# Performance work log

Measured on AMD Instinct MI355X. Metric: run time of the kernel, lower is better.

## Reference

```python
import jax, jax.numpy as jnp
import numpy as np

B, H, W, C, NH, K = 1, 64, 64, 384, 6, 7
DH = C // NH
EPS = 1e-6


def setup_inputs() -> dict:
    key = jax.random.key(0)
    ks = jax.random.split(key, 8)
    s = 0.02
    return {
        "x": jax.random.normal(ks[0], (B, H * W, C), jnp.float32),
        "cond": jax.random.normal(ks[1], (B, C), jnp.float32),
        "qkv_w": jax.random.normal(ks[2], (C, 3 * C), jnp.float32) * s,
        "qkv_b": jnp.zeros((3 * C,), jnp.float32),
        "proj_w": jax.random.normal(ks[3], (C, C), jnp.float32) * s,
        "proj_b": jnp.zeros((C,), jnp.float32),
        "fc1_w": jax.random.normal(ks[4], (C, 4 * C), jnp.float32) * s,
        "fc1_b": jnp.zeros((4 * C,), jnp.float32),
        "fc2_w": jax.random.normal(ks[5], (4 * C, C), jnp.float32) * s,
        "fc2_b": jnp.zeros((C,), jnp.float32),
        "ada_w": jax.random.normal(ks[6], (C, 6 * C), jnp.float32) * s,
        "ada_b": jnp.zeros((6 * C,), jnp.float32),
    }


def _ln(x):
    # LayerNorm with elementwise_affine=False, eps=1e-6
    mu = jnp.mean(x, axis=-1, keepdims=True)
    var = jnp.mean(jnp.square(x - mu), axis=-1, keepdims=True)
    return (x - mu) / jnp.sqrt(var + EPS)


def _win_idx(n):
    # NATTEN boundary-clamped window: start = clip(i - K//2, 0, n-K)
    starts = jnp.clip(jnp.arange(n) - K // 2, 0, n - K)
    return starts[:, None] + jnp.arange(K)[None, :]  # [n, K]


def _natten(y, qkv_w, qkv_b, proj_w, proj_b):
    # y: [B, H, W, C] -> neighborhood attention with 7x7 clamped windows
    qkv = y @ qkv_w + qkv_b
    q, k, v = jnp.split(qkv, 3, axis=-1)
    q = q.reshape(B, H, W, NH, DH) * (DH ** -0.5)
    k = k.reshape(B, H, W, NH, DH)
    v = v.reshape(B, H, W, NH, DH)
    ih = _win_idx(H)  # [H, K]
    iw = _win_idx(W)  # [W, K]
    kw = k[:, ih][:, :, :, iw]  # [B, H, K, W, K, NH, DH]
    vw = v[:, ih][:, :, :, iw]  # [B, H, K, W, K, NH, DH]
    a = jnp.einsum('bxynd,bxiyjnd->bxynij', q, kw)  # [B,H,W,NH,K,K]
    p = jax.nn.softmax(a.reshape(B, H, W, NH, K * K), axis=-1)
    p = p.reshape(B, H, W, NH, K, K)
    o = jnp.einsum('bxynij,bxiyjnd->bxynd', p, vw).reshape(B, H, W, C)
    return o @ proj_w + proj_b


def reference(x, cond, qkv_w, qkv_b, proj_w, proj_b,
              fc1_w, fc1_b, fc2_w, fc2_b, ada_w, ada_b):
    m = jax.nn.silu(cond) @ ada_w + ada_b  # [B, 6C]
    sh_a, sc_a, g_a, sh_m, sc_m, g_m = jnp.split(m, 6, axis=-1)
    # attention branch
    y = _ln(x) * (1.0 + sc_a[:, None]) + sh_a[:, None]
    z = _natten(y.reshape(B, H, W, C), qkv_w, qkv_b, proj_w, proj_b)
    x = x + g_a[:, None] * z.reshape(B, H * W, C)
    # mlp branch
    y = _ln(x) * (1.0 + sc_m[:, None]) + sh_m[:, None]
    hdn = jax.nn.gelu(y @ fc1_w + fc1_b, approximate=True)
    x = x + g_m[:, None] * (hdn @ fc2_w + fc2_b)
    return x
```

## Files before the change

### kernel.cpp

```cpp
#include <hip/hip_runtime.h>
#include <hip/hip_bf16.h>
#include <math.h>

#define GH 64
#define GW 64
#define CC 384
#define NHD 6
#define KW 7
#define DH 64
#define NTOK (GH*GW)
#define LN_EPS 1e-6f

typedef __attribute__((ext_vector_type(4))) float f32x4;
typedef __attribute__((ext_vector_type(8))) short bf16x8;
typedef __hip_bfloat16 bf16;

typedef const __attribute__((address_space(1))) unsigned int* gptr_t;
typedef __attribute__((address_space(3))) unsigned int* lptr_t;

__device__ __forceinline__ float bf2f(unsigned int u16) {
    union { unsigned int i; float f; } c; c.i = u16 << 16; return c.f;
}
__device__ __forceinline__ bf16 f2bf(float f) { return __float2bfloat16(f); }

__global__ __launch_bounds__(256) void wt_ada_k(const float* __restrict__ qkv_w,
                                                const float* __restrict__ proj_w,
                                                const float* __restrict__ fc1_w,
                                                const float* __restrict__ fc2_w,
                                                bf16* __restrict__ qkv_wt,
                                                bf16* __restrict__ proj_wt,
                                                bf16* __restrict__ fc1_wt,
                                                bf16* __restrict__ fc2_wt,
                                                const float* __restrict__ cond,
                                                const float* __restrict__ aw,
                                                const float* __restrict__ ab,
                                                float* __restrict__ m)
{
    int b = blockIdx.x;
    int tid = threadIdx.x;
    if (b >= 432) {
        __shared__ float s[CC];
        __shared__ float red[4][64];
        for (int i = tid; i < CC; i += 256) {
            float c = cond[i];
            s[i] = c / (1.f + __expf(-c));
        }
        __syncthreads();
        int c  = tid & 63;
        int ks = tid >> 6;
        int col = (b - 432) * 64 + c;
        float acc = 0.f;
        for (int k = ks * 96; k < (ks + 1) * 96; ++k)
            acc += s[k] * aw[(size_t)k * (6*CC) + col];
        red[ks][c] = acc;
        __syncthreads();
        if (tid < 64)
            m[col] = red[0][c] + red[1][c] + red[2][c] + red[3][c] + ab[col];
        return;
    }
    __shared__ float t[64][65];
    const float* in; bf16* outp; int K, N, lid;
    if (b < 108)       { in = qkv_w;  outp = qkv_wt;  K = 384;  N = 1152; lid = b; }
    else if (b < 144)  { in = proj_w; outp = proj_wt; K = 384;  N = 384;  lid = b - 108; }
    else if (b < 288)  { in = fc1_w;  outp = fc1_wt;  K = 384;  N = 1536; lid = b - 144; }
    else               { in = fc2_w;  outp = fc2_wt;  K = 1536; N = 384;  lid = b - 288; }
    int nbn = N >> 6;
    int bn = (lid % nbn) << 6, bk = (lid / nbn) << 6;
    int c4 = (tid & 15) * 4, r0 = tid >> 4;
    #pragma unroll
    for (int p = 0; p < 4; ++p) {
        int r = r0 + p * 16;
        float4 v = *(const float4*)&in[(size_t)(bk + r) * N + bn + c4];
        t[r][c4+0] = v.x; t[r][c4+1] = v.y; t[r][c4+2] = v.z; t[r][c4+3] = v.w;
    }
    __syncthreads();
    #pragma unroll
    for (int p = 0; p < 4; ++p) {
        int n = r0 + p * 16;
        ushort4 w;
        w.x = __bfloat16_as_ushort(f2bf(t[c4+0][n]));
        w.y = __bfloat16_as_ushort(f2bf(t[c4+1][n]));
        w.z = __bfloat16_as_ushort(f2bf(t[c4+2][n]));
        w.w = __bfloat16_as_ushort(f2bf(t[c4+3][n]));
        *(ushort4*)&outp[(size_t)(bn + n) * K + bk + c4] = w;
    }
}

__global__ __launch_bounds__(128) void ln_mod_k(const float* __restrict__ xin,
                                                const float* __restrict__ sh,
                                                const float* __restrict__ sc,
                                                bf16* __restrict__ yout)
{
    int t = blockIdx.x;
    int tid = threadIdx.x;
    const float* xr = xin + (size_t)t * CC;
    float v0 = xr[tid], v1 = xr[tid + 128], v2 = xr[tid + 256];
    float s  = v0 + v1 + v2;
    float ss = v0*v0 + v1*v1 + v2*v2;
    #pragma unroll
    for (int off = 32; off; off >>= 1) {
        s  += __shfl_down(s,  off);
        ss += __shfl_down(ss, off);
    }
    __shared__ float red[4];
    int wid = tid >> 6;
    if ((tid & 63) == 0) { red[wid*2] = s; red[wid*2+1] = ss; }
    __syncthreads();
    s  = red[0] + red[2];
    ss = red[1] + red[3];
    float mean = s * (1.f / CC);
    float var  = ss * (1.f / CC) - mean * mean;
    float rstd = rsqrtf(var + LN_EPS);
    bf16* yr = yout + (size_t)t * CC;
    yr[tid      ] = f2bf((v0 - mean) * rstd * (1.f + sc[tid      ]) + sh[tid      ]);
    yr[tid + 128] = f2bf((v1 - mean) * rstd * (1.f + sc[tid + 128]) + sh[tid + 128]);
    yr[tid + 256] = f2bf((v2 - mean) * rstd * (1.f + sc[tid + 256]) + sh[tid + 256]);
}

#define GBK 64

template<int EPI, typename OutT, int BM, int BN, int TPB, int DEPTH>
__global__ __launch_bounds__(TPB) void mgemm_k(const bf16* __restrict__ A,
                                               const bf16* __restrict__ Bt,
                                               const float* __restrict__ bias,
                                               const float* __restrict__ resid,
                                               const float* __restrict__ gvec,
                                               OutT* __restrict__ out,
                                               int M, int N, int Kd)
{
    constexpr int WR = 2, WC = TPB / 128;
    constexpr int FM = BM / WR / 16, FN = BN / WC / 16;
    constexpr int RPP = TPB / 8;
    constexpr int PA = BM / RPP > 0 ? BM / RPP : 1;
    constexpr int PB = BN / RPP > 0 ? BN / RPP : 1;
    constexpr int LDST = PA + PB;
    constexpr int STAGE_BYTES = DEPTH * (BM + BN) * GBK * 2;
    constexpr int EPI_BYTES = (EPI == 1) ? BM * (BN + 4) * 4 : BM * (BN + 8) * 2;
    constexpr int SMEM = STAGE_BYTES > EPI_BYTES ? STAGE_BYTES : EPI_BYTES;
    __shared__ __align__(16) char smem[SMEM];
    bf16* As = (bf16*)smem;
    bf16* Bs = (bf16*)(smem + DEPTH * BM * GBK * 2);

    int tid = threadIdx.x;
    int wid = tid >> 6, lane = tid & 63;
    int wm = wid / WC, wn = wid % WC;

    int gx = gridDim.x;
    int nwg = gx * gridDim.y;
    int bid = blockIdx.y * gx + blockIdx.x;
    int swz = (bid & 7) * (nwg >> 3) + (bid >> 3);
    int bx = swz % gx, by = swz / gx;

    int row_base = by * BM;
    int col_base = bx * BN;

    int l8 = lane >> 3;
    int cs = ((lane & 7) ^ l8) * 8;
    int xr = (lane & 7) << 4;
    int bcol = (lane >> 4) * 16;

    f32x4 acc[FM][FN] = {};
    const int nt = Kd / GBK;

    auto STAGE = [&](int buf, int t) {
        int k0 = t * GBK;
        #pragma unroll
        for (int p = 0; p < PA; ++p) {
            int rb = (p * RPP + wid * 8) % BM;
            __builtin_amdgcn_global_load_lds(
                (gptr_t)(const void*)(A + (size_t)(row_base + rb + l8) * Kd + k0 + cs),
                (lptr_t)(void*)(As + (buf * BM + rb) * GBK), 16, 0, 0);
        }
        #pragma unroll
        for (int p = 0; p < PB; ++p) {
            int rb = (p * RPP + wid * 8) % BN;
            __builtin_amdgcn_global_load_lds(
                (gptr_t)(const void*)(Bt + (size_t)(col_base + rb + l8) * Kd + k0 + cs),
                (lptr_t)(void*)(Bs + (buf * BN + rb) * GBK), 16, 0, 0);
        }
    };

    #pragma unroll
    for (int d = 0; d < DEPTH - 1; ++d) STAGE(d, d);

    int cur = 0;
    for (int t = 0; t < nt; ++t) {
        if (t + DEPTH - 1 < nt)
            STAGE((cur + DEPTH - 1) % DEPTH, t + DEPTH - 1);
        int ahead = min(nt - 1, t + DEPTH - 1) - t;
        if constexpr (DEPTH == 3) {
            if (ahead == 2)      asm volatile("s_waitcnt vmcnt(%0)" :: "n"(2*LDST) : "memory");
            else if (ahead == 1) asm volatile("s_waitcnt vmcnt(%0)" :: "n"(LDST)   : "memory");
            else                 asm volatile("s_waitcnt vmcnt(0)" ::: "memory");
        } else {
            if (ahead == 1)      asm volatile("s_waitcnt vmcnt(%0)" :: "n"(LDST)   : "memory");
            else                 asm volatile("s_waitcnt vmcnt(0)" ::: "memory");
        }
        __builtin_amdgcn_sched_barrier(0);
        __builtin_amdgcn_s_barrier();
        __builtin_amdgcn_sched_barrier(0);
        #pragma unroll
        for (int kk = 0; kk < GBK; kk += 32) {
            bf16x8 af[FM], bfr[FN];
            #pragma unroll
            for (int m = 0; m < FM; ++m) {
                int R = wm*(BM/WR) + m*16 + (lane & 15);
                af[m]  = *(const bf16x8*)((const char*)As + (cur*BM + R)*128 + ((kk*2 + bcol) ^ xr));
            }
            #pragma unroll
            for (int n = 0; n < FN; ++n) {
                int R = wn*(BN/WC) + n*16 + (lane & 15);
                bfr[n] = *(const bf16x8*)((const char*)Bs + (cur*BN + R)*128 + ((kk*2 + bcol) ^ xr));
            }
            #pragma unroll
            for (int m = 0; m < FM; ++m)
                #pragma unroll
                for (int n = 0; n < FN; ++n)
                    acc[m][n] = __builtin_amdgcn_mfma_f32_16x16x32_bf16(af[m], bfr[n], acc[m][n], 0, 0, 0);
        }
        __builtin_amdgcn_sched_barrier(0);
        __builtin_amdgcn_s_barrier();
        __builtin_amdgcn_sched_barrier(0);
        cur = (cur + 1 == DEPTH) ? 0 : cur + 1;
    }

    int cl = lane & 15, rq = lane >> 4;
    if constexpr (EPI == 1) {
        float* et = (float*)smem;
        #pragma unroll
        for (int m = 0; m < FM; ++m)
            #pragma unroll
            for (int n = 0; n < FN; ++n) {
                int col = wn*(BN/WC) + n*16 + cl;
                float bv = bias[col_base + col];
                #pragma unroll
                for (int j = 0; j < 4; ++j) {
                    int row = wm*(BM/WR) + m*16 + rq*4 + j;
                    et[row*(BN+4) + col] = acc[m][n][j] + bv;
                }
            }
        __syncthreads();
        constexpr int CH = BN / 4;
        #pragma unroll
        for (int p = 0; p < (BM*CH)/TPB; ++p) {
            int idx = p * TPB + tid;
            int row = idx / CH, ch = idx % CH;
            float4 v = *(const float4*)&et[row*(BN+4) + ch*4];
            size_t gidx = (size_t)(row_base + row) * N + col_base + ch*4;
            float4 r = *(const float4*)&resid[gidx];
            float4 g = *(const float4*)&gvec[col_base + ch*4];
            float4 o;
            o.x = r.x + g.x * v.x;
            o.y = r.y + g.y * v.y;
            o.z = r.z + g.z * v.z;
            o.w = r.w + g.w * v.w;
            *(float4*)&((float*)out)[gidx] = o;
        }
    } else {
        bf16* et = (bf16*)smem;
        #pragma unroll
        for (int m = 0; m < FM; ++m)
            #pragma unroll
            for (int n = 0; n < FN; ++n) {
                int col = wn*(BN/WC) + n*16 + cl;
                float bv = bias[col_base + col];
                #pragma unroll
                for (int j = 0; j < 4; ++j) {
                    int row = wm*(BM/WR) + m*16 + rq*4 + j;
                    float v = acc[m][n][j] + bv;
                    if constexpr (EPI == 2) {
                        float u = 0.7978845608028654f * (v + 0.044715f * v * v * v);
                        v = v / (1.f + __expf(-2.f * u));
                    }
                    et[row*(BN+8) + col] = f2bf(v);
                }
            }
        __syncthreads();
        constexpr int CH = BN / 8;
        #pragma unroll
        for (int p = 0; p < (BM*CH)/TPB; ++p) {
            int idx = p * TPB + tid;
            int row = idx / CH, ch = idx % CH;
            bf16x8 v = *(const bf16x8*)&et[row*(BN+8) + ch*8];
            *(bf16x8*)&((bf16*)out)[(size_t)(row_base + row) * N + col_base + ch*8] = v;
        }
    }
}

#define QOFF 0
#define KOFF 8192
#define VOFF 36864
#define POFF 65536

__global__ __launch_bounds__(256) void natten_k(const bf16* __restrict__ qkv,
                                                bf16* __restrict__ o)
{
    __shared__ __align__(16) char lds[95232];
    int tid = threadIdx.x;
    int wid = tid >> 6, lane = tid & 63;
    int b = blockIdx.x;
    int h = b % NHD, tile = b / NHD;
    int R0 = (tile >> 3) << 3, C0 = (tile & 7) << 3;
    int wr0 = min(max(R0 - 3, 0), GH - 14);
    int wc0 = min(max(C0 - 3, 0), GW - 14);

    int l8 = lane >> 3, c8 = lane & 7;
    int cs = ((c8 ^ l8) << 3);

    #pragma unroll
    for (int p = 0; p < 2; ++p) {
        int rb = p * 32 + wid * 8;
        int q  = rb + l8;
        int token = (R0 + (q >> 3)) * GW + C0 + (q & 7);
        __builtin_amdgcn_global_load_lds(
            (gptr_t)(const void*)(qkv + (size_t)token * (3*CC) + h * DH + cs),
            (lptr_t)(void*)(lds + QOFF + rb * 128), 16, 0, 0);
    }
    #pragma unroll
    for (int p = 0; p < 7; ++p) {
        int rb = p * 32 + wid * 8;
        int key = rb + l8;
        if (key < 196) {
            int kr = (key * 586) >> 13;
            int kc = key - 14 * kr;
            int token = (wr0 + kr) * GW + wc0 + kc;
            const bf16* base = qkv + (size_t)token * (3*CC) + h * DH + cs;
            __builtin_amdgcn_global_load_lds(
                (gptr_t)(const void*)(base + CC),
                (lptr_t)(void*)(lds + KOFF + rb * 128), 16, 0, 0);
            __builtin_amdgcn_global_load_lds(
                (gptr_t)(const void*)(base + 2*CC),
                (lptr_t)(void*)(lds + VOFF + rb * 128), 16, 0, 0);
        }
    }
    for (int i = tid; i < 896; i += 256)
        *(unsigned int*)(lds + VOFF + 196*128 + i * 4) = 0u;
    for (int i = tid; i < 64*18; i += 256) {
        int row = i / 18, seg = i % 18;
        *(unsigned int*)(lds + POFF + row * 464 + 392 + seg * 4) = 0u;
    }
    __syncthreads();

    int qme = wid * 16 + (lane & 15);
    int qr = R0 + (qme >> 3), qc = C0 + (qme & 7);
    int sh = min(max(qr - 3, 0), GH - KW);
    int sw = min(max(qc - 3, 0), GW - KW);

    bf16x8 bq[2];
    #pragma unroll
    for (int kk = 0; kk < 2; ++kk)
        bq[kk] = *(const bf16x8*)(lds + QOFF + qme * 128 +
                  ((kk * 64 + (lane >> 4) * 16) ^ ((qme & 7) << 4)));

    f32x4 sc[13] = {};
    #pragma unroll
    for (int m = 0; m < 13; ++m) {
        #pragma unroll
        for (int kk = 0; kk < 2; ++kk) {
            int R = m * 16 + (lane & 15);
            bf16x8 af = *(const bf16x8*)(lds + KOFF + R * 128 +
                         ((kk * 64 + (lane >> 4) * 16) ^ ((R & 7) << 4)));
            sc[m] = __builtin_amdgcn_mfma_f32_16x16x32_bf16(af, bq[kk], sc[m], 0, 0, 0);
        }
    }
    float mx = -3e38f;
    #pragma unroll
    for (int m = 0; m < 13; ++m) {
        #pragma unroll
        for (int j = 0; j < 4; ++j) {
            int key = m * 16 + (lane >> 4) * 4 + j;
            int kr = (key * 586) >> 13;
            int kc = key - 14 * kr;
            int kg = wr0 + kr, cg = wc0 + kc;
            bool val = (kg >= sh) && (kg <= sh + 6) && (cg >= sw) && (cg <= sw + 6);
            float s = val ? sc[m][j] * 0.125f : -3e38f;
            sc[m][j] = s;
            mx = fmaxf(mx, s);
        }
    }
    mx = fmaxf(mx, __shfl_xor(mx, 16));
    mx = fmaxf(mx, __shfl_xor(mx, 32));
    float sum = 0.f;
    #pragma unroll
    for (int m = 0; m < 13; ++m)
        #pragma unroll
        for (int j = 0; j < 4; ++j) {
            float e = __expf(sc[m][j] - mx);
            sc[m][j] = e;
            sum += e;
        }
    sum += __shfl_xor(sum, 16);
    sum += __shfl_xor(sum, 32);
    float inv = 1.f / sum;

    #pragma unroll
    for (int m = 0; m < 13; ++m)
        #pragma unroll
        for (int j = 0; j < 4; ++j) {
            int key = m * 16 + (lane >> 4) * 4 + j;
            *(bf16*)(lds + POFF + qme * 464 + key * 2) = f2bf(sc[m][j]);
        }
    asm volatile("s_waitcnt lgkmcnt(0)" ::: "memory");
    __builtin_amdgcn_sched_barrier(0);

    f32x4 oacc[4] = {};
    #pragma unroll
    for (int kk = 0; kk < 7; ++kk) {
        bf16x8 af = *(const bf16x8*)(lds + POFF + qme * 464 + kk * 64 + (lane >> 4) * 16);
        #pragma unroll
        for (int n = 0; n < 4; ++n) {
            int dd = n * 16 + (lane & 15);
            int gch = dd >> 3, dby = (dd & 7) * 2;
            bf16x8 bv;
            #pragma unroll
            for (int j = 0; j < 8; ++j) {
                int key = kk * 32 + (lane >> 4) * 8 + j;
                ((short*)&bv)[j] = *(const short*)(lds + VOFF + key * 128 +
                                    ((gch ^ (key & 7)) << 4) + dby);
            }
            oacc[n] = __builtin_amdgcn_mfma_f32_16x16x32_bf16(af, bv, oacc[n], 0, 0, 0);
        }
    }

    #pragma unroll
    for (int j = 0; j < 4; ++j) {
        int idxq = ((lane >> 4) << 2) + j;
        float iv = __shfl(inv, (lane & 48) | idxq);
        int q2 = wid * 16 + idxq;
        int token = (R0 + (q2 >> 3)) * GW + C0 + (q2 & 7);
        #pragma unroll
        for (int n = 0; n < 4; ++n) {
            int d = n * 16 + (lane & 15);
            o[(size_t)token * CC + h * DH + d] = f2bf(oacc[n][j] * iv);
        }
    }
}

extern "C" void kernel_launch(void* const* d_in, const int* in_sizes, int n_in,
                              void* d_out, int out_size, void* d_ws, size_t ws_size,
                              hipStream_t stream)
{
    const float* x      = (const float*)d_in[0];
    const float* cond   = (const float*)d_in[1];
    const float* qkv_w  = (const float*)d_in[2];
    const float* qkv_b  = (const float*)d_in[3];
    const float* proj_w = (const float*)d_in[4];
    const float* proj_b = (const float*)d_in[5];
    const float* fc1_w  = (const float*)d_in[6];
    const float* fc1_b  = (const float*)d_in[7];
    const float* fc2_w  = (const float*)d_in[8];
    const float* fc2_b  = (const float*)d_in[9];
    const float* ada_w  = (const float*)d_in[10];
    const float* ada_b  = (const float*)d_in[11];
    float* out = (float*)d_out;

    char* p = (char*)d_ws;
    float* m       = (float*)p;            p += 6*CC*sizeof(float);
    bf16* y        = (bf16*)p;             p += (size_t)NTOK*CC*2;
    bf16* qkv      = (bf16*)p;             p += (size_t)NTOK*(3*CC)*2;
    bf16* attn_o   = (bf16*)p;             p += (size_t)NTOK*CC*2;
    bf16* hdn      = (bf16*)p;             p += (size_t)NTOK*(4*CC)*2;
    bf16* qkv_wt   = (bf16*)p;             p += (size_t)(3*CC)*CC*2;
    bf16* proj_wt  = (bf16*)p;             p += (size_t)CC*CC*2;
    bf16* fc1_wt   = (bf16*)p;             p += (size_t)(4*CC)*CC*2;
    bf16* fc2_wt   = (bf16*)p;             p += (size_t)CC*(4*CC)*2;

    const float* sh_a = m;
    const float* sc_a = m + CC;
    const float* g_a  = m + 2*CC;
    const float* sh_m = m + 3*CC;
    const float* sc_m = m + 4*CC;
    const float* g_m  = m + 5*CC;

    wt_ada_k<<<468, 256, 0, stream>>>(qkv_w, proj_w, fc1_w, fc2_w,
                                      qkv_wt, proj_wt, fc1_wt, fc2_wt,
                                      cond, ada_w, ada_b, m);
    ln_mod_k<<<NTOK, 128, 0, stream>>>(x, sh_a, sc_a, y);
    mgemm_k<0, bf16, 64, 128, 256, 2><<<dim3((3*CC)/128, NTOK/64), 256, 0, stream>>>(
        y, qkv_wt, qkv_b, nullptr, nullptr, qkv, NTOK, 3*CC, CC);
    natten_k<<<(NTOK/64)*NHD, 256, 0, stream>>>(qkv, attn_o);
    mgemm_k<1, float, 32, 64, 256, 3><<<dim3(CC/64, NTOK/32), 256, 0, stream>>>(
        attn_o, proj_wt, proj_b, x, g_a, out, NTOK, CC, CC);
    ln_mod_k<<<NTOK, 128, 0, stream>>>(out, sh_m, sc_m, y);
    mgemm_k<2, bf16, 64, 128, 256, 2><<<dim3((4*CC)/128, NTOK/64), 256, 0, stream>>>(
        y, fc1_wt, fc1_b, nullptr, nullptr, hdn, NTOK, 4*CC, CC);
    mgemm_k<1, float, 32, 64, 256, 3><<<dim3(CC/64, NTOK/32), 256, 0, stream>>>(
        hdn, fc2_wt, fc2_b, out, g_m, out, NTOK, CC, 4*CC);
}
```

Measured before the change: 79.84 us.

## Fold first LayerNorm into front kernel and apply adaLN modulation inside GEMM A-loads

The first LayerNorm no longer depends on the adaLN vector, so it now runs inside the weight-transpose/ada kernel as extra blocks, which removes one launch and lets it overlap with the weight conversion. Scale and shift are applied to A fragments in registers inside the qkv and fc1 GEMMs, using a shared-memory copy of the modulation vector. The second LayerNorm now handles two tokens per block. The trade is extra per-fragment bf16 unpack/FMA/repack work in the GEMM inner loop, a second bf16 rounding of the activations, and a redundant double load of the modulation values.

Result: slower. 82.58 us (+3.4%).

```diff
diff --git a/kernel.cpp b/kernel.cpp
--- a/kernel.cpp
+++ b/kernel.cpp
@@ -23,24 +23,55 @@
 }
 __device__ __forceinline__ bf16 f2bf(float f) { return __float2bfloat16(f); }
 
-__global__ __launch_bounds__(256) void wt_ada_k(const float* __restrict__ qkv_w,
-                                                const float* __restrict__ proj_w,
-                                                const float* __restrict__ fc1_w,
-                                                const float* __restrict__ fc2_w,
-                                                bf16* __restrict__ qkv_wt,
-                                                bf16* __restrict__ proj_wt,
-                                                bf16* __restrict__ fc1_wt,
-                                                bf16* __restrict__ fc2_wt,
-                                                const float* __restrict__ cond,
-                                                const float* __restrict__ aw,
-                                                const float* __restrict__ ab,
-                                                float* __restrict__ m)
+__global__ __launch_bounds__(256) void front_k(const float* __restrict__ qkv_w,
+                                               const float* __restrict__ proj_w,
+                                               const float* __restrict__ fc1_w,
+                                               const float* __restrict__ fc2_w,
+                                               bf16* __restrict__ qkv_wt,
+                                               bf16* __restrict__ proj_wt,
+                                               bf16* __restrict__ fc1_wt,
+                                               bf16* __restrict__ fc2_wt,
+                                               const float* __restrict__ cond,
+                                               const float* __restrict__ aw,
+                                               const float* __restrict__ ab,
+                                               float* __restrict__ m,
+                                               const float* __restrict__ x,
+                                               bf16* __restrict__ z)
 {
+    __shared__ float t[64][65];
     int b = blockIdx.x;
     int tid = threadIdx.x;
+    if (b >= 468) {
+        int tok = (b - 468) * 2 + (tid >> 7);
+        int lt  = tid & 127;
+        const float* xr = x + (size_t)tok * CC;
+        float v0 = xr[lt], v1 = xr[lt + 128], v2 = xr[lt + 256];
+        float s  = v0 + v1 + v2;
+        float ss = v0*v0 + v1*v1 + v2*v2;
+        #pragma unroll
+        for (int off = 32; off; off >>= 1) {
+            s  += __shfl_down(s,  off);
+            ss += __shfl_down(ss, off);
+        }
+        float* red = (float*)t;
+        int wid = tid >> 6;
+        if ((tid & 63) == 0) { red[wid*2] = s; red[wid*2+1] = ss; }
+        __syncthreads();
+        int base = (tid >> 7) * 4;
+        s  = red[base+0] + red[base+2];
+        ss = red[base+1] + red[base+3];
+        float mean = s * (1.f / CC);
+        float var  = ss * (1.f / CC) - mean * mean;
+        float rstd = rsqrtf(var + LN_EPS);
+        bf16* zr = z + (size_t)tok * CC;
+        zr[lt      ] = f2bf((v0 - mean) * rstd);
+        zr[lt + 128] = f2bf((v1 - mean) * rstd);
+        zr[lt + 256] = f2bf((v2 - mean) * rstd);
+        return;
+    }
     if (b >= 432) {
-        __shared__ float s[CC];
-        __shared__ float red[4][64];
+        float* s   = (float*)t;
+        float* red = s + CC;
         for (int i = tid; i < CC; i += 256) {
             float c = cond[i];
             s[i] = c / (1.f + __expf(-c));
@@ -52,13 +83,12 @@
         float acc = 0.f;
         for (int k = ks * 96; k < (ks + 1) * 96; ++k)
             acc += s[k] * aw[(size_t)k * (6*CC) + col];
-        red[ks][c] = acc;
+        red[ks*64 + c] = acc;
         __syncthreads();
         if (tid < 64)
-            m[col] = red[0][c] + red[1][c] + red[2][c] + red[3][c] + ab[col];
+            m[col] = red[c] + red[64+c] + red[128+c] + red[192+c] + ab[col];
         return;
     }
-    __shared__ float t[64][65];
     const float* in; bf16* outp; int K, N, lid;
     if (b < 108)       { in = qkv_w;  outp = qkv_wt;  K = 384;  N = 1152; lid = b; }
     else if (b < 144)  { in = proj_w; outp = proj_wt; K = 384;  N = 384;  lid = b - 108; }
@@ -86,15 +116,13 @@
     }
 }
 
-__global__ __launch_bounds__(128) void ln_mod_k(const float* __restrict__ xin,
-                                                const float* __restrict__ sh,
-                                                const float* __restrict__ sc,
-                                                bf16* __restrict__ yout)
+__global__ __launch_bounds__(256) void ln_k(const float* __restrict__ xin,
+                                            bf16* __restrict__ z)
 {
-    int t = blockIdx.x;
-    int tid = threadIdx.x;
-    const float* xr = xin + (size_t)t * CC;
-    float v0 = xr[tid], v1 = xr[tid + 128], v2 = xr[tid + 256];
+    int tok = blockIdx.x * 2 + (threadIdx.x >> 7);
+    int lt  = threadIdx.x & 127;
+    const float* xr = xin + (size_t)tok * CC;
+    float v0 = xr[lt], v1 = xr[lt + 128], v2 = xr[lt + 256];
     float s  = v0 + v1 + v2;
     float ss = v0*v0 + v1*v1 + v2*v2;
     #pragma unroll
@@ -102,29 +130,31 @@
         s  += __shfl_down(s,  off);
         ss += __shfl_down(ss, off);
     }
-    __shared__ float red[4];
-    int wid = tid >> 6;
-    if ((tid & 63) == 0) { red[wid*2] = s; red[wid*2+1] = ss; }
+    __shared__ float red[8];
+    int wid = threadIdx.x >> 6;
+    if ((threadIdx.x & 63) == 0) { red[wid*2] = s; red[wid*2+1] = ss; }
     __syncthreads();
-    s  = red[0] + red[2];
-    ss = red[1] + red[3];
+    int base = (threadIdx.x >> 7) * 4;
+    s  = red[base+0] + red[base+2];
+    ss = red[base+1] + red[base+3];
     float mean = s * (1.f / CC);
     float var  = ss * (1.f / CC) - mean * mean;
     float rstd = rsqrtf(var + LN_EPS);
-    bf16* yr = yout + (size_t)t * CC;
-    yr[tid      ] = f2bf((v0 - mean) * rstd * (1.f + sc[tid      ]) + sh[tid      ]);
-    yr[tid + 128] = f2bf((v1 - mean) * rstd * (1.f + sc[tid + 128]) + sh[tid + 128]);
-    yr[tid + 256] = f2bf((v2 - mean) * rstd * (1.f + sc[tid + 256]) + sh[tid + 256]);
+    bf16* zr = z + (size_t)tok * CC;
+    zr[lt      ] = f2bf((v0 - mean) * rstd);
+    zr[lt + 128] = f2bf((v1 - mean) * rstd);
+    zr[lt + 256] = f2bf((v2 - mean) * rstd);
 }
 
 #define GBK 64
 
-template<int EPI, typename OutT, int BM, int BN, int TPB, int DEPTH>
+template<int EPI, int MOD, typename OutT, int BM, int BN, int TPB, int DEPTH>
 __global__ __launch_bounds__(TPB) void mgemm_k(const bf16* __restrict__ A,
                                                const bf16* __restrict__ Bt,
                                                const float* __restrict__ bias,
                                                const float* __restrict__ resid,
                                                const float* __restrict__ gvec,
+                                               const float* __restrict__ modv,
                                                OutT* __restrict__ out,
                                                int M, int N, int Kd)
 {
@@ -138,6 +168,7 @@
     constexpr int EPI_BYTES = (EPI == 1) ? BM * (BN + 4) * 4 : BM * (BN + 8) * 2;
     constexpr int SMEM = STAGE_BYTES > EPI_BYTES ? STAGE_BYTES : EPI_BYTES;
     __shared__ __align__(16) char smem[SMEM];
+    __shared__ __align__(16) float smod[MOD ? 2*CC : 4];
     bf16* As = (bf16*)smem;
     bf16* Bs = (bf16*)(smem + DEPTH * BM * GBK * 2);
 
@@ -161,6 +192,14 @@
 
     f32x4 acc[FM][FN] = {};
     const int nt = Kd / GBK;
+
+    if constexpr (MOD) {
+        for (int i = tid; i < CC; i += TPB) {
+            smod[i]      = modv[i];
+            smod[CC + i] = 1.f + modv[CC + i];
+        }
+        __syncthreads();
+    }
 
     auto STAGE = [&](int buf, int t) {
         int k0 = t * GBK;
@@ -203,9 +242,35 @@
         for (int kk = 0; kk < GBK; kk += 32) {
             bf16x8 af[FM], bfr[FN];
             #pragma unroll
-            for (int m = 0; m < FM; ++m) {
-                int R = wm*(BM/WR) + m*16 + (lane & 15);
-                af[m]  = *(const bf16x8*)((const char*)As + (cur*BM + R)*128 + ((kk*2 + bcol) ^ xr));
+            for (int m2 = 0; m2 < FM; ++m2) {
+                int R = wm*(BM/WR) + m2*16 + (lane & 15);
+                af[m2] = *(const bf16x8*)((const char*)As + (cur*BM + R)*128 + ((kk*2 + bcol) ^ xr));
+            }
+            if constexpr (MOD) {
+                int kg = ((kk*2 + bcol) >> 1);
+                float s0a[8], s1a[8];
+                *(f32x4*)&s0a[0] = *(const f32x4*)&smod[kg];
+                *(f32x4*)&s0a[4] = *(const f32x4*)&smod[kg + 4];
+                *(f32x4*)&s1a[0] = *(const f32x4*)&smod[CC + kg];
+                *(f32x4*)&s1a[4] = *(const f32x4*)&smod[CC + kg + 4];
+                if (t > 0) {
+                    int kgg = t * GBK + kg;
+                    *(f32x4*)&s0a[0] = *(const f32x4*)&smod[kgg];
+                    *(f32x4*)&s0a[4] = *(const f32x4*)&smod[kgg + 4];
+                    *(f32x4*)&s1a[0] = *(const f32x4*)&smod[CC + kgg];
+                    *(f32x4*)&s1a[4] = *(const f32x4*)&smod[CC + kgg + 4];
+                }
+                #pragma unroll
+                for (int m2 = 0; m2 < FM; ++m2) {
+                    bf16x8 v = af[m2];
+                    #pragma unroll
+                    for (int i = 0; i < 8; ++i) {
+                        float f = bf2f((unsigned short)v[i]);
+                        f = f * s1a[i] + s0a[i];
+                        v[i] = (short)__bfloat16_as_ushort(f2bf(f));
+                    }
+                    af[m2] = v;
+                }
             }
             #pragma unroll
             for (int n = 0; n < FN; ++n) {
@@ -213,10 +278,10 @@
                 bfr[n] = *(const bf16x8*)((const char*)Bs + (cur*BN + R)*128 + ((kk*2 + bcol) ^ xr));
             }
             #pragma unroll
-            for (int m = 0; m < FM; ++m)
+            for (int m2 = 0; m2 < FM; ++m2)
                 #pragma unroll
                 for (int n = 0; n < FN; ++n)
-                    acc[m][n] = __builtin_amdgcn_mfma_f32_16x16x32_bf16(af[m], bfr[n], acc[m][n], 0, 0, 0);
+                    acc[m2][n] = __builtin_amdgcn_mfma_f32_16x16x32_bf16(af[m2], bfr[n], acc[m2][n], 0, 0, 0);
         }
         __builtin_amdgcn_sched_barrier(0);
         __builtin_amdgcn_s_barrier();
@@ -228,15 +293,15 @@
     if constexpr (EPI == 1) {
         float* et = (float*)smem;
         #pragma unroll
-        for (int m = 0; m < FM; ++m)
+        for (int m2 = 0; m2 < FM; ++m2)
             #pragma unroll
             for (int n = 0; n < FN; ++n) {
                 int col = wn*(BN/WC) + n*16 + cl;
                 float bv = bias[col_base + col];
                 #pragma unroll
                 for (int j = 0; j < 4; ++j) {
-                    int row = wm*(BM/WR) + m*16 + rq*4 + j;
-                    et[row*(BN+4) + col] = acc[m][n][j] + bv;
+                    int row = wm*(BM/WR) + m2*16 + rq*4 + j;
+                    et[row*(BN+4) + col] = acc[m2][n][j] + bv;
                 }
             }
         __syncthreads();
@@ -259,15 +324,15 @@
     } else {
         bf16* et = (bf16*)smem;
         #pragma unroll
-        for (int m = 0; m < FM; ++m)
+        for (int m2 = 0; m2 < FM; ++m2)
             #pragma unroll
             for (int n = 0; n < FN; ++n) {
                 int col = wn*(BN/WC) + n*16 + cl;
                 float bv = bias[col_base + col];
                 #pragma unroll
                 for (int j = 0; j < 4; ++j) {
-                    int row = wm*(BM/WR) + m*16 + rq*4 + j;
-                    float v = acc[m][n][j] + bv;
+                    int row = wm*(BM/WR) + m2*16 + rq*4 + j;
+                    float v = acc[m2][n][j] + bv;
                     if constexpr (EPI == 2) {
                         float u = 0.7978845608028654f * (v + 0.044715f * v * v * v);
                         v = v / (1.f + __expf(-2.f * u));
@@ -465,25 +530,20 @@
     bf16* fc1_wt   = (bf16*)p;             p += (size_t)(4*CC)*CC*2;
     bf16* fc2_wt   = (bf16*)p;             p += (size_t)CC*(4*CC)*2;
 
-    const float* sh_a = m;
-    const float* sc_a = m + CC;
     const float* g_a  = m + 2*CC;
-    const float* sh_m = m + 3*CC;
-    const float* sc_m = m + 4*CC;
     const float* g_m  = m + 5*CC;
 
-    wt_ada_k<<<468, 256, 0, stream>>>(qkv_w, proj_w, fc1_w, fc2_w,
+    front_k<<<2516, 256, 0, stream>>>(qkv_w, proj_w, fc1_w, fc2_w,
                                       qkv_wt, proj_wt, fc1_wt, fc2_wt,
-                                      cond, ada_w, ada_b, m);
-    ln_mod_k<<<NTOK, 128, 0, stream>>>(x, sh_a, sc_a, y);
-    mgemm_k<0, bf16, 64, 128, 256, 2><<<dim3((3*CC)/128, NTOK/64), 256, 0, stream>>>(
-        y, qkv_wt, qkv_b, nullptr, nullptr, qkv, NTOK, 3*CC, CC);
+                                      cond, ada_w, ada_b, m, x, y);
+    mgemm_k<0, 1, bf16, 64, 128, 256, 2><<<dim3((3*CC)/128, NTOK/64), 256, 0, stream>>>(
+        y, qkv_wt, qkv_b, nullptr, nullptr, m, qkv, NTOK, 3*CC, CC);
     natten_k<<<(NTOK/64)*NHD, 256, 0, stream>>>(qkv, attn_o);
-    mgemm_k<1, float, 32, 64, 256, 3><<<dim3(CC/64, NTOK/32), 256, 0, stream>>>(
-        attn_o, proj_wt, proj_b, x, g_a, out, NTOK, CC, CC);
-    ln_mod_k<<<NTOK, 128, 0, stream>>>(out, sh_m, sc_m, y);
-    mgemm_k<2, bf16, 64, 128, 256, 2><<<dim3((4*CC)/128, NTOK/64), 256, 0, stream>>>(
-        y, fc1_wt, fc1_b, nullptr, nullptr, hdn, NTOK, 4*CC, CC);
-    mgemm_k<1, float, 32, 64, 256, 3><<<dim3(CC/64, NTOK/32), 256, 0, stream>>>(
-        hdn, fc2_wt, fc2_b, out, g_m, out, NTOK, CC, 4*CC);
+    mgemm_k<1, 0, float, 32, 64, 256, 3><<<dim3(CC/64, NTOK/32), 256, 0, stream>>>(
+        attn_o, proj_wt, proj_b, x, g_a, nullptr, out, NTOK, CC, CC);
+    ln_k<<<NTOK/2, 256, 0, stream>>>(out, y);
+    mgemm_k<2, 1, bf16, 64, 128, 256, 2><<<dim3((4*CC)/128, NTOK/64), 256, 0, stream>>>(
+        y, fc1_wt, fc1_b, nullptr, nullptr, m + 3*CC, hdn, NTOK, 4*CC, CC);
+    mgemm_k<1, 0, float, 32, 64, 256, 3><<<dim3(CC/64, NTOK/32), 256, 0, stream>>>(
+        hdn, fc2_wt, fc2_b, out, g_m, nullptr, out, NTOK, CC, 4*CC);
 }
```

## Fuse second LayerNorm-modulate into proj GEMM epilogue via last-block counter

Applied to the files above, without the earlier changes.

Removes the separate ln_mod_k launch after the attention projection. Each proj GEMM block atomically increments a per-row-tile counter, and the last block to finish a 32-row tile computes the LayerNorm and modulation for those rows and writes the bf16 input of fc1. This saves one kernel launch and one pass over the fp32 residual. In exchange it adds threadfences and atomics, and the tail block does serialized LN work while the other blocks of that row tile sit idle.

Result: slower. 174.0 us (+117.9%).

```diff
diff --git a/kernel.cpp b/kernel.cpp
--- a/kernel.cpp
+++ b/kernel.cpp
@@ -34,10 +34,12 @@
                                                 const float* __restrict__ cond,
                                                 const float* __restrict__ aw,
                                                 const float* __restrict__ ab,
-                                                float* __restrict__ m)
+                                                float* __restrict__ m,
+                                                int* __restrict__ cnt)
 {
     int b = blockIdx.x;
     int tid = threadIdx.x;
+    if (b == 0 && tid < 128) cnt[tid] = 0;
     if (b >= 432) {
         __shared__ float s[CC];
         __shared__ float red[4][64];
@@ -119,12 +121,15 @@
 
 #define GBK 64
 
-template<int EPI, typename OutT, int BM, int BN, int TPB, int DEPTH>
+template<int EPI, int LNF, typename OutT, int BM, int BN, int TPB, int DEPTH>
 __global__ __launch_bounds__(TPB) void mgemm_k(const bf16* __restrict__ A,
                                                const bf16* __restrict__ Bt,
                                                const float* __restrict__ bias,
                                                const float* __restrict__ resid,
                                                const float* __restrict__ gvec,
+                                               const float* __restrict__ modv,
+                                               bf16* __restrict__ yout,
+                                               int* __restrict__ cnt,
                                                OutT* __restrict__ out,
                                                int M, int N, int Kd)
 {
@@ -203,9 +208,9 @@
         for (int kk = 0; kk < GBK; kk += 32) {
             bf16x8 af[FM], bfr[FN];
             #pragma unroll
-            for (int m = 0; m < FM; ++m) {
-                int R = wm*(BM/WR) + m*16 + (lane & 15);
-                af[m]  = *(const bf16x8*)((const char*)As + (cur*BM + R)*128 + ((kk*2 + bcol) ^ xr));
+            for (int m2 = 0; m2 < FM; ++m2) {
+                int R = wm*(BM/WR) + m2*16 + (lane & 15);
+                af[m2] = *(const bf16x8*)((const char*)As + (cur*BM + R)*128 + ((kk*2 + bcol) ^ xr));
             }
             #pragma unroll
             for (int n = 0; n < FN; ++n) {
@@ -213,10 +218,10 @@
                 bfr[n] = *(const bf16x8*)((const char*)Bs + (cur*BN + R)*128 + ((kk*2 + bcol) ^ xr));
             }
             #pragma unroll
-            for (int m = 0; m < FM; ++m)
+            for (int m2 = 0; m2 < FM; ++m2)
                 #pragma unroll
                 for (int n = 0; n < FN; ++n)
-                    acc[m][n] = __builtin_amdgcn_mfma_f32_16x16x32_bf16(af[m], bfr[n], acc[m][n], 0, 0, 0);
+                    acc[m2][n] = __builtin_amdgcn_mfma_f32_16x16x32_bf16(af[m2], bfr[n], acc[m2][n], 0, 0, 0);
         }
         __builtin_amdgcn_sched_barrier(0);
         __builtin_amdgcn_s_barrier();
@@ -228,15 +233,15 @@
     if constexpr (EPI == 1) {
         float* et = (float*)smem;
         #pragma unroll
-        for (int m = 0; m < FM; ++m)
+        for (int m2 = 0; m2 < FM; ++m2)
             #pragma unroll
             for (int n = 0; n < FN; ++n) {
                 int col = wn*(BN/WC) + n*16 + cl;
                 float bv = bias[col_base + col];
                 #pragma unroll
                 for (int j = 0; j < 4; ++j) {
-                    int row = wm*(BM/WR) + m*16 + rq*4 + j;
-                    et[row*(BN+4) + col] = acc[m][n][j] + bv;
+                    int row = wm*(BM/WR) + m2*16 + rq*4 + j;
+                    et[row*(BN+4) + col] = acc[m2][n][j] + bv;
                 }
             }
         __syncthreads();
@@ -256,18 +261,67 @@
             o.w = r.w + g.w * v.w;
             *(float4*)&((float*)out)[gidx] = o;
         }
+        if constexpr (LNF) {
+            __threadfence();
+            __shared__ int lastf;
+            if (tid == 0) {
+                int old = atomicAdd(&cnt[by], 1);
+                lastf = (old == (int)gridDim.x - 1);
+                if (lastf) atomicExch(&cnt[by], 0);
+            }
+            __syncthreads();
+            if (!lastf) return;
+            __threadfence();
+            int r  = tid >> 3;
+            int sg = tid & 7;
+            const float* x1 = (const float*)out + (size_t)(row_base + r) * CC + sg * 48;
+            float s = 0.f, ss = 0.f;
+            #pragma unroll
+            for (int c = 0; c < 48; c += 4) {
+                float4 v = *(const float4*)&x1[c];
+                s  += v.x + v.y + v.z + v.w;
+                ss += v.x*v.x + v.y*v.y + v.z*v.z + v.w*v.w;
+            }
+            #pragma unroll
+            for (int off = 1; off < 8; off <<= 1) {
+                s  += __shfl_xor(s,  off);
+                ss += __shfl_xor(ss, off);
+            }
+            float mean = s * (1.f / CC);
+            float rstd = rsqrtf(ss * (1.f / CC) - mean * mean + LN_EPS);
+            bf16* yr = yout + (size_t)(row_base + r) * CC + sg * 48;
+            #pragma unroll
+            for (int c = 0; c < 48; c += 8) {
+                float4 va = *(const float4*)&x1[c];
+                float4 vb = *(const float4*)&x1[c + 4];
+                float4 ha = *(const float4*)&modv[sg*48 + c];
+                float4 hb = *(const float4*)&modv[sg*48 + c + 4];
+                float4 ca = *(const float4*)&modv[CC + sg*48 + c];
+                float4 cb = *(const float4*)&modv[CC + sg*48 + c + 4];
+                bf16x8 w;
+                w[0] = (short)__bfloat16_as_ushort(f2bf((va.x-mean)*rstd*(1.f+ca.x)+ha.x));
+                w[1] = (short)__bfloat16_as_ushort(f2bf((va.y-mean)*rstd*(1.f+ca.y)+ha.y));
+                w[2] = (short)__bfloat16_as_ushort(f2bf((va.z-mean)*rstd*(1.f+ca.z)+ha.z));
+                w[3] = (short)__bfloat16_as_ushort(f2bf((va.w-mean)*rstd*(1.f+ca.w)+ha.w));
+                w[4] = (short)__bfloat16_as_ushort(f2bf((vb.x-mean)*rstd*(1.f+cb.x)+hb.x));
+                w[5] = (short)__bfloat16_as_ushort(f2bf((vb.y-mean)*rstd*(1.f+cb.y)+hb.y));
+                w[6] = (short)__bfloat16_as_ushort(f2bf((vb.z-mean)*rstd*(1.f+cb.z)+hb.z));
+                w[7] = (short)__bfloat16_as_ushort(f2bf((vb.w-mean)*rstd*(1.f+cb.w)+hb.w));
+                *(bf16x8*)&yr[c] = w;
+            }
+        }
     } else {
         bf16* et = (bf16*)smem;
         #pragma unroll
-        for (int m = 0; m < FM; ++m)
+        for (int m2 = 0; m2 < FM; ++m2)
             #pragma unroll
             for (int n = 0; n < FN; ++n) {
                 int col = wn*(BN/WC) + n*16 + cl;
                 float bv = bias[col_base + col];
                 #pragma unroll
                 for (int j = 0; j < 4; ++j) {
-                    int row = wm*(BM/WR) + m*16 + rq*4 + j;
-                    float v = acc[m][n][j] + bv;
+                    int row = wm*(BM/WR) + m2*16 + rq*4 + j;
+                    float v = acc[m2][n][j] + bv;
                     if constexpr (EPI == 2) {
                         float u = 0.7978845608028654f * (v + 0.044715f * v * v * v);
                         v = v / (1.f + __expf(-2.f * u));
@@ -464,26 +518,28 @@
     bf16* proj_wt  = (bf16*)p;             p += (size_t)CC*CC*2;
     bf16* fc1_wt   = (bf16*)p;             p += (size_t)(4*CC)*CC*2;
     bf16* fc2_wt   = (bf16*)p;             p += (size_t)CC*(4*CC)*2;
+    int*  cnt      = (int*)p;              p += 128*sizeof(int);
 
     const float* sh_a = m;
     const float* sc_a = m + CC;
     const float* g_a  = m + 2*CC;
-    const float* sh_m = m + 3*CC;
-    const float* sc_m = m + 4*CC;
     const float* g_m  = m + 5*CC;
 
     wt_ada_k<<<468, 256, 0, stream>>>(qkv_w, proj_w, fc1_w, fc2_w,
                                       qkv_wt, proj_wt, fc1_wt, fc2_wt,
-                                      cond, ada_w, ada_b, m);
+                                      cond, ada_w, ada_b, m, cnt);
     ln_mod_k<<<NTOK, 128, 0, stream>>>(x, sh_a, sc_a, y);
-    mgemm_k<0, bf16, 64, 128, 256, 2><<<dim3((3*CC)/128, NTOK/64), 256, 0, stream>>>(
-        y, qkv_wt, qkv_b, nullptr, nullptr, qkv, NTOK, 3*CC, CC);
+    mgemm_k<0, 0, bf16, 64, 128, 256, 2><<<dim3((3*CC)/128, NTOK/64), 256, 0, stream>>>(
+        y, qkv_wt, qkv_b, nullptr, nullptr, nullptr, nullptr, nullptr,
+        qkv, NTOK, 3*CC, CC);
     natten_k<<<(NTOK/64)*NHD, 256, 0, stream>>>(qkv, attn_o);
-    mgemm_k<1, float, 32, 64, 256, 3><<<dim3(CC/64, NTOK/32), 256, 0, stream>>>(
-        attn_o, proj_wt, proj_b, x, g_a, out, NTOK, CC, CC);
-    ln_mod_k<<<NTOK, 128, 0, stream>>>(out, sh_m, sc_m, y);
-    mgemm_k<2, bf16, 64, 128, 256, 2><<<dim3((4*CC)/128, NTOK/64), 256, 0, stream>>>(
-        y, fc1_wt, fc1_b, nullptr, nullptr, hdn, NTOK, 4*CC, CC);
-    mgemm_k<1, float, 32, 64, 256, 3><<<dim3(CC/64, NTOK/32), 256, 0, stream>>>(
-        hdn, fc2_wt, fc2_b, out, g_m, out, NTOK, CC, 4*CC);
+    mgemm_k<1, 1, float, 32, 64, 256, 3><<<dim3(CC/64, NTOK/32), 256, 0, stream>>>(
+        attn_o, proj_wt, proj_b, x, g_a, m + 3*CC, y, cnt,
+        out, NTOK, CC, CC);
+    mgemm_k<2, 0, bf16, 64, 128, 256, 2><<<dim3((4*CC)/128, NTOK/64), 256, 0, stream>>>(
+        y, fc1_wt, fc1_b, nullptr, nullptr, nullptr, nullptr, nullptr,
+        hdn, NTOK, 4*CC, CC);
+    mgemm_k<1, 0, float, 32, 64, 256, 3><<<dim3(CC/64, NTOK/32), 256, 0, stream>>>(
+        hdn, fc2_wt, fc2_b, out, g_m, nullptr, nullptr, nullptr,
+        out, NTOK, CC, 4*CC);
 }
```
